# Performance work log

Hardware: AMD Instinct MI355X
Metric: run time of the kernel (lower is better)

## Reference

```python
import jax, jax.numpy as jnp
import numpy as np
import math

B, C, H, W = 512, 64, 8, 8
E, NH, MEM = 64, 8, 8          # embed_dim, num_heads, mem_n
HD = E // NH                   # head_dim
THD = H * W * HD               # tot_head_dim = 512
AMB = 5.0                      # attn_mask_b
LN_EPS = 1e-5


def conv2d(x, w, b):
    y = jax.lax.conv_general_dilated(x, w, (1, 1), 'SAME',
                                     dimension_numbers=('NCHW', 'OIHW', 'NCHW'))
    return y + b[None, :, None, None]


def setup_inputs() -> dict:
    key = jax.random.key(0)
    ks = jax.random.split(key, 14)
    r = lambda k, s, sc=1.0: jax.random.normal(k, s, dtype=jnp.float32) * sc
    return {
        'input': r(ks[0], (B, C, H, W)),
        'h_cur': r(ks[1], (B, E, H, W)),
        'c_cur': r(ks[2], (B, E, H, W)),
        'concat_k': r(ks[3], (B, MEM, NH, THD)),
        'concat_v': r(ks[4], (B, MEM, NH, THD)),
        'attn_mask': jax.random.randint(ks[5], (B * NH, 1, MEM), 0, 2).astype(bool),
        'conv_w': r(ks[6], (5 * E, C + E, 3, 3), 0.05),
        'conv_b': jnp.zeros((5 * E,), jnp.float32),
        'proj_w': r(ks[7], (3 * E, C, 3, 3), 0.05),
        'proj_b': jnp.zeros((3 * E,), jnp.float32),
        'out_w': r(ks[8], (E, E, 3, 3), 0.05),
        'out_b': jnp.zeros((E,), jnp.float32),
        'ln_w': jnp.ones((E, H, W), jnp.float32),
        'ln_b': jnp.zeros((E, H, W), jnp.float32),
        'pos_w': r(ks[9], (MEM, H * W * E), 0.02),
        'pos_b': jax.random.uniform(ks[10], (MEM, NH), jnp.float32, -0.1, 0.1),
    }


def _cell(input, h_cur, c_cur, concat_k, concat_v, attn_mask,
          conv_w, conv_b, proj_w, proj_b, out_w, out_b, ln_w, ln_b, pos_w, pos_b):
    # ConvLSTM gates
    combined = jnp.concatenate([input, h_cur], axis=1)          # [B, C+E, H, W]
    cc = conv2d(combined, conv_w, conv_b)                       # [B, 5E, H, W]
    cc_i, cc_f, cc_o, cc_g, cc_a = jnp.split(cc, 5, axis=1)
    i = jax.nn.sigmoid(cc_i)
    f = jax.nn.sigmoid(cc_f)
    o = jax.nn.sigmoid(cc_o)
    g = jnp.tanh(cc_g)
    a = jax.nn.sigmoid(cc_a)
    c_next = f * c_cur + i * g

    # attention over growing memory
    kqv = conv2d(input, proj_w, proj_b)                         # [B, 3E, H, W]
    k, q, v = jnp.split(kqv, 3, axis=1)
    # [B, E, H, W] -> [B*NH, 1, THD] (contiguous split of E into NH heads)
    resh = lambda x: x.reshape(B * NH, 1, THD)
    k, q, v = resh(k), resh(q), resh(v)
    q_scaled = q / math.sqrt(THD)

    # prior memory: [B, MEM, NH, THD] -> [B*NH, MEM-1, THD]
    def mem_resh(m):
        return jnp.transpose(m[:, 1:], (1, 0, 2, 3)).reshape(MEM - 1, B * NH, THD).transpose(1, 0, 2)
    k_full = jnp.concatenate([mem_resh(concat_k), k], axis=1)   # [B*NH, MEM, THD]
    v_full = jnp.concatenate([mem_resh(concat_v), v], axis=1)

    # learned positional key offsets / score biases
    pos_w_e = jnp.broadcast_to(pos_w[:, None, :], (MEM, B, H * W * E)) \
                 .reshape(MEM, B * NH, THD).transpose(1, 0, 2)  # [B*NH, MEM, THD]
    pos_b_e = jnp.broadcast_to(pos_b[:, None, :], (MEM, B, NH)) \
                 .reshape(MEM, B * NH).T                        # [B*NH, MEM]
    k_full = k_full + pos_w_e

    # additive mask: -inf where masked, last slot forced to +attn_mask_b
    mask = jnp.where(attn_mask, -jnp.inf, 0.0).astype(q.dtype)  # [B*NH, 1, MEM]
    mask = mask.at[:, :, -1].set(AMB)

    scores = mask + jnp.einsum('bqd,bkd->bqk', q_scaled, k_full) + pos_b_e[:, None, :]
    w = jax.nn.softmax(scores, axis=-1)                         # [B*NH, 1, MEM]
    attn = jnp.einsum('bqk,bkd->bqd', w, v_full)                # [B*NH, 1, THD]
    attn = attn.reshape(B, E, H, W)

    out = conv2d(attn, out_w, out_b) + input[:, :E]
    # LayerNorm over (E, H, W)
    mu = jnp.mean(out, axis=(1, 2, 3), keepdims=True)
    var = jnp.mean((out - mu) ** 2, axis=(1, 2, 3), keepdims=True)
    out = (out - mu) / jnp.sqrt(var + LN_EPS) * ln_w[None] + ln_b[None]

    c_next = c_next + a * jnp.tanh(out)
    h_next = o * jnp.tanh(c_next)

    ret = lambda m: m.transpose(1, 0, 2).reshape(MEM, B, NH, THD).transpose(1, 0, 2, 3)
    return h_next, c_next, ret(k_full), ret(v_full)


def reference(input, h_cur, c_cur, concat_k, concat_v, attn_mask,
              conv_w, conv_b, proj_w, proj_b, out_w, out_b, ln_w, ln_b, pos_w, pos_b):
    return _cell(input, h_cur, c_cur, concat_k, concat_v, attn_mask,
                 conv_w, conv_b, proj_w, proj_b, out_w, out_b, ln_w, ln_b, pos_w, pos_b)
```

## Files before the change

### kernel.cpp

```cpp
#include <hip/hip_runtime.h>

typedef short short8 __attribute__((ext_vector_type(8)));
typedef __bf16 bf16x8 __attribute__((ext_vector_type(8)));
typedef float f32x4 __attribute__((ext_vector_type(4)));
typedef short s16x4 __attribute__((ext_vector_type(4)));
typedef unsigned u32x4 __attribute__((ext_vector_type(4)));

__device__ __forceinline__ short f2bf(float f) {
  unsigned u = __builtin_bit_cast(unsigned, f);
  u = (u + 0x7FFFu + ((u >> 16) & 1u)) >> 16;
  return (short)u;
}
__device__ __forceinline__ f32x4 mfma16(short8 a, short8 b, f32x4 c) {
  return __builtin_amdgcn_mfma_f32_16x16x32_bf16(
      __builtin_bit_cast(bf16x8, a), __builtin_bit_cast(bf16x8, b), c, 0, 0, 0);
}
__device__ __forceinline__ float sigm(float x) { return 1.0f / (1.0f + __expf(-x)); }
__device__ __forceinline__ float ftanh(float x) {
  return 1.0f - 2.0f / (1.0f + __expf(2.0f * x));
}
__device__ __forceinline__ f32x4 ld4(const float* p) { return *(const f32x4*)p; }
__device__ __forceinline__ void ntst4(float* p, f32x4 v) {
  __builtin_nontemporal_store(v, (f32x4*)p);
}
// ... 25 lines not shown
    }
    *(short8*)&out[(46080 + e) * 8] = v;
    return;
  }
  e -= 13824;
  {
    int kb8 = e / 64, n = e % 64;
    short8 v;
#pragma unroll
    for (int j = 0; j < 8; ++j) {
      int k = kb8 * 8 + j;
      int tap = k >> 6, ci = k & 63;
      v[j] = f2bf(w3[(n * 64 + ci) * 9 + tap]);
    }
    *(short8*)&out[(46080 + 13824 + e) * 8] = v;
  }
}

__launch_bounds__(512, 4)
__global__ void mid2_k(const float* __restrict__ input, const float* __restrict__ h_cur,
                       const float* __restrict__ c_cur, const float* __restrict__ ck,
                       const int* __restrict__ amask,
                       const float* __restrict__ conv_b, const float* __restrict__ proj_b,
                       const float* __restrict__ pos_w, const float* __restrict__ pos_b,
                       const short* __restrict__ pk1, const short* __restrict__ pk2,
                       float* __restrict__ o_k, float* __restrict__ o_v,
                       float* __restrict__ ws_wt, float* __restrict__ ws_ct,
                       unsigned* __restrict__ ws_oa) {
  __shared__ short comb[12800];
  __shared__ float Xb[4160];
  __shared__ float Vx[4160];
  __shared__ float sc_lds[8];
  float* combf = (float*)comb;
  unsigned* Xbu = (unsigned*)Xb;

  const int tid = threadIdx.x;
  const int wave = tid >> 6, lane = tid & 63;
  const int col = lane & 15, g4 = lane >> 4;
  const int wc = wave >> 1, wm = wave & 1;
  const int ch = wc * 16 + col;

  if (blockIdx.x < 512) {
    const int b = blockIdx.x;
    const int hd = wave;
    const int d0 = lane * 4, d1 = (lane + 64) * 4;
    if (tid < 8) sc_lds[tid] = 0.f;

#pragma unroll
    for (int i = 0; i < 2; ++i) {
      int idx = (tid + 512 * i) * 4;
      int c = idx >> 6, p0 = idx & 63;
      f32x4 vi = ld4(&input[b * 4096 + idx]);
#pragma unroll
      for (int j = 0; j < 4; ++j) {
        int p = p0 + j;
        int pp = ((p >> 3) + 1) * 10 + (p & 7) + 1;
        comb[pp * 64 + ((c + pp * 8) & 63)] = f2bf(vi[j]);
      }
    }
    for (int i = tid; i < 2304; i += 512) {
      int pr = i >> 6, c = i & 63;
      int pp = (pr < 10) ? pr
               : (pr < 20) ? (80 + pr)
               : (pr < 28) ? ((pr - 19) * 10)
                           : ((pr - 27) * 10 + 9);
      comb[pp * 64 + c] = 0;
    }
    __syncthreads();

    f32x4 acc2[2][3];
#pragma unroll
    for (int m = 0; m < 2; ++m)
#pragma unroll
      for (int g = 0; g < 3; ++g) acc2[m][g] = (f32x4){0.f, 0.f, 0.f, 0.f};
    short8 bb2[3];
#pragma unroll
    for (int g = 0; g < 3; ++g)
      bb2[g] = *(const short8*)&pk2[((g4)*192 + g * 64 + ch) * 8];
    for (int s = 0; s < 18; ++s) {
      short8 bbn[3];
      if (s < 17) {
        int kb8 = (s + 1) * 4 + g4;
#pragma unroll
        for (int g = 0; g < 3; ++g)
          bbn[g] = *(const short8*)&pk2[(kb8 * 192 + g * 64 + ch) * 8];
      }
      int tap = s >> 1, cib = s & 1;
      int kh = tap / 3, kw = tap % 3;
      short8 a[2];
#pragma unroll
      for (int m = 0; m < 2; ++m) {
        int p = (wm * 2 + m) * 16 + col;
        int pp = ((p >> 3) + kh) * 10 + (p & 7) + kw;
        int slot = (cib * 32 + g4 * 8 + pp * 8) & 63;
        a[m] = *(const short8*)&comb[pp * 64 + slot];
      }
#pragma unroll
      for (int m = 0; m < 2; ++m)
#pragma unroll
        for (int g = 0; g < 3; ++g) acc2[m][g] = mfma16(a[m], bb2[g], acc2[m][g]);
      if (s < 17) {
#pragma unroll
        for (int g = 0; g < 3; ++g) bb2[g] = bbn[g];
      }
    }

    float kreg[8], qreg[8], vreg[8], part7 = 0.f;
    {
      float pb0 = proj_b[ch], pb1 = proj_b[64 + ch], pb2 = proj_b[128 + ch];
      const float rsq = 0.044194173824159216f;
#pragma unroll
      for (int m = 0; m < 2; ++m)
#pragma unroll
        for (int r = 0; r < 4; ++r) {
          int p = (wm * 2 + m) * 16 + g4 * 4 + r;
          float kf = acc2[m][0][r] + pb0 + pos_w[7 * 4096 + ch * 64 + p];
          float qf = (acc2[m][1][r] + pb1) * rsq;
          float vf = acc2[m][2][r] + pb2;
          kreg[m * 4 + r] = kf;
          qreg[m * 4 + r] = qf;
          vreg[m * 4 + r] = vf;
          part7 = fmaf(qf, kf, part7);
        }
    }
    atomicAdd(&sc_lds[ch >> 3], part7);

    int msks[7];
    float pbv[7];
#pragma unroll
    for (int m = 0; m < 7; ++m) {
      msks[m] = amask[(b * 8 + hd) * 8 + m];
      pbv[m] = pos_b[m * 8 + hd];
    }

    __syncthreads();

#pragma unroll
    for (int m = 0; m < 2; ++m)
#pragma unroll
      for (int r = 0; r < 4; ++r) {
        int p = (wm * 2 + m) * 16 + g4 * 4 + r;
        combf[ch * 65 + p] = kreg[m * 4 + r];
        Xb[ch * 65 + p] = qreg[m * 4 + r];
        Vx[ch * 65 + p] = vreg[m * 4 + r];
      }
    __syncthreads();

    const size_t base7 = (size_t)(b * 64 + 56) * 512;
#pragma unroll
    for (int i = 0; i < 2; ++i) {
      int idx = (tid + 512 * i) * 4;
      int c = idx >> 6, p0 = idx & 63;
      f32x4 kq, vq;
#pragma unroll
      for (int j = 0; j < 4; ++j) {
        kq[j] = combf[c * 65 + p0 + j];
        vq[j] = Vx[c * 65 + p0 + j];
      }
      ntst4(&o_k[base7 + idx], kq);
      *(f32x4*)&o_v[base7 + idx] = vq;
    }
    const int cs0 = d0 >> 6, po0 = d0 & 63, cs1 = d1 >> 6, po1 = d1 & 63;
    f32x4 q0, q1;
#pragma unroll
    for (int j = 0; j < 4; ++j) {
      q0[j] = Xb[(hd * 8 + cs0) * 65 + po0 + j];
      q1[j] = Xb[(hd * 8 + cs1) * 65 + po1 + j];
    }
    float sc7 = sc_lds[hd] + pos_b[7 * 8 + hd] + 5.0f;

    float scv[8];
    scv[7] = sc7;
#pragma unroll
    for (int m = 0; m < 7; ++m) {
      const float* kp = ck + ((size_t)((b * 8 + m + 1) * 8 + hd)) * 512;
      const float* pw = pos_w + m * 4096 + hd * 512;
      f32x4 k0 = ld4(kp + d0) + ld4(pw + d0);
      f32x4 k1 = ld4(kp + d1) + ld4(pw + d1);
      float* dst = o_k + ((size_t)((b * 8 + m) * 8 + hd)) * 512;
      ntst4(dst + d0, k0);
      ntst4(dst + d1, k1);
      float part = 0.f;
#pragma unroll
      for (int j = 0; j < 4; ++j) {
        part = fmaf(q0[j], k0[j], part);
        part = fmaf(q1[j], k1[j], part);
      }
#pragma unroll
      for (int off = 32; off >= 1; off >>= 1) part += __shfl_xor(part, off);
      scv[m] = part + pbv[m] + (msks[m] ? -__builtin_inff() : 0.0f);
    }

    float mx = scv[0];
#pragma unroll
    for (int m = 1; m < 8; ++m) mx = fmaxf(mx, scv[m]);
    float w[8], s = 0.f;
#pragma unroll
    for (int m = 0; m < 8; ++m) {
      w[m] = __expf(scv[m] - mx);
      s += w[m];
    }
    float inv = 1.0f / s;
    if (lane == 0) {
#pragma unroll
      for (int m = 0; m < 8; ++m)
        ws_wt[(size_t)b * 64 + hd * 8 + m] = w[m] * inv;
    }
  } else {
    const int b = blockIdx.x - 512;
#pragma unroll
    for (int i = 0; i < 2; ++i) {
      int idx = (tid + 512 * i) * 4;
      int c = idx >> 6, p0 = idx & 63;
      f32x4 vi = ld4(&input[b * 4096 + idx]);
      f32x4 vh = ld4(&h_cur[b * 4096 + idx]);
      f32x4 vc = ld4(&c_cur[b * 4096 + idx]);
#pragma unroll
      for (int j = 0; j < 4; ++j) {
        int p = p0 + j;
        int pp = ((p >> 3) + 1) * 10 + (p & 7) + 1;
        comb[pp * 128 + ((c + pp * 8) & 127)] = f2bf(vi[j]);
        comb[pp * 128 + ((c + 64 + pp * 8) & 127)] = f2bf(vh[j]);
        Xb[c * 65 + p] = vc[j];
      }
    }
    for (int i = tid; i < 4608; i += 512) {
      int pr = i >> 7, c = i & 127;
      int pp = (pr < 10) ? pr
               : (pr < 20) ? (80 + pr)
               : (pr < 28) ? ((pr - 19) * 10)
                           : ((pr - 27) * 10 + 9);
      comb[pp * 128 + c] = 0;
    }
    __syncthreads();

    f32x4 acc1[2][5];
#pragma unroll
    for (int m = 0; m < 2; ++m)
#pragma unroll
      for (int g = 0; g < 5; ++g) acc1[m][g] = (f32x4){0.f, 0.f, 0.f, 0.f};
    short8 bb1[5];
#pragma unroll
    for (int g = 0; g < 5; ++g)
      bb1[g] = *(const short8*)&pk1[((g4)*320 + g * 64 + ch) * 8];
    for (int s = 0; s < 36; ++s) {
      short8 bbn[5];
      if (s < 35) {
        int kb8 = (s + 1) * 4 + g4;
#pragma unroll
        for (int g = 0; g < 5; ++g)
          bbn[g] = *(const short8*)&pk1[(kb8 * 320 + g * 64 + ch) * 8];
      }
      int tap = s >> 2, cib = s & 3;
      int kh = tap / 3, kw = tap % 3;
      short8 a[2];
#pragma unroll
      for (int m = 0; m < 2; ++m) {
        int p = (wm * 2 + m) * 16 + col;
        int pp = ((p >> 3) + kh) * 10 + (p & 7) + kw;
        int slot = (cib * 32 + g4 * 8 + pp * 8) & 127;
        a[m] = *(const short8*)&comb[pp * 128 + slot];
      }
#pragma unroll
      for (int m = 0; m < 2; ++m)
#pragma unroll
        for (int g = 0; g < 5; ++g) acc1[m][g] = mfma16(a[m], bb1[g], acc1[m][g]);
      if (s < 35) {
#pragma unroll
        for (int g = 0; g < 5; ++g) bb1[g] = bbn[g];
      }
    }

    float ctv[8];
    unsigned oav[8];
    {
      float bi0 = conv_b[ch], bi1 = conv_b[64 + ch], bi2 = conv_b[128 + ch];
      float bi3 = conv_b[192 + ch], bi4 = conv_b[256 + ch];
#pragma unroll
      for (int m = 0; m < 2; ++m)
#pragma unroll
        for (int r = 0; r < 4; ++r) {
          int p = (wm * 2 + m) * 16 + g4 * 4 + r;
          float iv = sigm(acc1[m][0][r] + bi0);
          float fv = sigm(acc1[m][1][r] + bi1);
          float ov = sigm(acc1[m][2][r] + bi2);
          float gv = ftanh(acc1[m][3][r] + bi3);
          float av = sigm(acc1[m][4][r] + bi4);
          ctv[m * 4 + r] = fv * Xb[ch * 65 + p] + iv * gv;
          oav[m * 4 + r] = ((unsigned)(unsigned short)f2bf(av) << 16) |
                           (unsigned)(unsigned short)f2bf(ov);
        }
    }
    __syncthreads();
#pragma unroll
    for (int m = 0; m < 2; ++m)
#pragma unroll
      for (int r = 0; r < 4; ++r) {
        int p = (wm * 2 + m) * 16 + g4 * 4 + r;
        combf[ch * 65 + p] = ctv[m * 4 + r];
        Xbu[ch * 65 + p] = oav[m * 4 + r];
      }
    __syncthreads();
#pragma unroll
    for (int i = 0; i < 2; ++i) {
      int idx = (tid + 512 * i) * 4;
      int c = idx >> 6, p0 = idx & 63;
      f32x4 cq;
      u32x4 oq;
#pragma unroll
      for (int j = 0; j < 4; ++j) {
        cq[j] = combf[c * 65 + p0 + j];
        oq[j] = Xbu[c * 65 + p0 + j];
      }
      *(f32x4*)&ws_ct[(size_t)b * 4096 + idx] = cq;
      *(u32x4*)&ws_oa[(size_t)b * 4096 + idx] = oq;
    }
  }
}

__launch_bounds__(512, 4)
__global__ void tail_k(const float* __restrict__ input, const float* __restrict__ cv,
                       const float* __restrict__ ws_wt,
                       const float* __restrict__ ws_ct,
                       const unsigned* __restrict__ ws_oa,
                       const float* __restrict__ out_b,
                       const float* __restrict__ ln_w, const float* __restrict__ ln_b,
                       const short* __restrict__ pk3,
                       float* __restrict__ o_h, float* __restrict__ o_c,
                       float* __restrict__ o_v) {
  __shared__ short comb[8320];
  __shared__ float Xb[4160];
  __shared__ float wt_s[64];
  __shared__ float red[16];
  float* combf = (float*)comb;
  unsigned* Xbu = (unsigned*)Xb;

  const int b = blockIdx.x;
  const int tid = threadIdx.x;
  const int wave = tid >> 6, lane = tid & 63;
  const int col = lane & 15, g4 = lane >> 4;
  const int wc = wave >> 1, wm = wave & 1;
  const int ch = wc * 16 + col;
  const int hd = wave;
  const int d0 = lane * 4, d1 = (lane + 64) * 4;

  f32x4 ctr[2];
  u32x4 oar[2];
#pragma unroll
  for (int i = 0; i < 2; ++i) {
    int idx = (tid + 512 * i) * 4;
    ctr[i] = ld4(&ws_ct[(size_t)b * 4096 + idx]);
    oar[i] = *(const u32x4*)&ws_oa[(size_t)b * 4096 + idx];
  }
  if (tid < 64) wt_s[tid] = ws_wt[(size_t)b * 64 + tid];

#pragma unroll
  for (int i = 0; i < 2; ++i) {
    int idx = (tid + 512 * i) * 4;
    int c = idx >> 6, p0 = idx & 63;
    f32x4 vi = ld4(&input[b * 4096 + idx]);
#pragma unroll
    for (int j = 0; j < 4; ++j) Xb[c * 65 + p0 + j] = vi[j];
  }
  for (int i = tid; i < 2304; i += 512) {
    int pr = i >> 6, c = i & 63;
    int pp = (pr < 10) ? pr
             : (pr < 20) ? (80 + pr)
             : (pr < 28) ? ((pr - 19) * 10)
                         : ((pr - 27) * 10 + 9);
    comb[pp * 64 + c] = 0;
  }
  __syncthreads();

  float wv[8];
#pragma unroll
  for (int m = 0; m < 8; ++m) wv[m] = wt_s[hd * 8 + m];

  f32x4 a0 = (f32x4){0.f, 0.f, 0.f, 0.f};
  f32x4 a1 = (f32x4){0.f, 0.f, 0.f, 0.f};
#pragma unroll
  for (int m = 0; m < 7; ++m) {
    const float* vp = cv + ((size_t)((b * 8 + m + 1) * 8 + hd)) * 512;
    f32x4 v0 = ld4(vp + d0);
    f32x4 v1 = ld4(vp + d1);
    float* dst = o_v + ((size_t)((b * 8 + m) * 8 + hd)) * 512;
    ntst4(dst + d0, v0);
    ntst4(dst + d1, v1);
    a0 += v0 * wv[m];
    a1 += v1 * wv[m];
  }
  {
    const float* vp = o_v + ((size_t)((b * 8 + 7) * 8 + hd)) * 512;
    a0 += ld4(vp + d0) * wv[7];
    a1 += ld4(vp + d1) * wv[7];
  }
#pragma unroll
  for (int j = 0; j < 4; ++j) {
    int dA = d0 + j, dB = d1 + j;
    int cA = hd * 8 + (dA >> 6), pA = dA & 63;
    int cB = hd * 8 + (dB >> 6), pB = dB & 63;
    int ppA = ((pA >> 3) + 1) * 10 + (pA & 7) + 1;
    int ppB = ((pB >> 3) + 1) * 10 + (pB & 7) + 1;
    comb[ppA * 64 + ((cA + ppA * 8) & 63)] = f2bf(a0[j]);
    comb[ppB * 64 + ((cB + ppB * 8) & 63)] = f2bf(a1[j]);
  }
  __syncthreads();

  f32x4 acc3[2];
  acc3[0] = (f32x4){0.f, 0.f, 0.f, 0.f};
  acc3[1] = (f32x4){0.f, 0.f, 0.f, 0.f};
  short8 bb3 = *(const short8*)&pk3[((g4)*64 + ch) * 8];
  for (int s = 0; s < 18; ++s) {
    short8 bbn;
    if (s < 17) {
      int kb8 = (s + 1) * 4 + g4;
      bbn = *(const short8*)&pk3[(kb8 * 64 + ch) * 8];
    }
    int tap = s >> 1, cib = s & 1;
    int kh = tap / 3, kw = tap % 3;
    short8 a[2];
#pragma unroll
    for (int m = 0; m < 2; ++m) {
      int p = (wm * 2 + m) * 16 + col;
      int pp = ((p >> 3) + kh) * 10 + (p & 7) + kw;
      int slot = (cib * 32 + g4 * 8 + pp * 8) & 63;
      a[m] = *(const short8*)&comb[pp * 64 + slot];
    }
#pragma unroll
    for (int m = 0; m < 2; ++m) acc3[m] = mfma16(a[m], bb3, acc3[m]);
    if (s < 17) bb3 = bbn;
  }

  float ov_[8], s1 = 0.f, s2 = 0.f;
  {
    float ob = out_b[ch];
#pragma unroll
    for (int m = 0; m < 2; ++m)
#pragma unroll
      for (int r = 0; r < 4; ++r) {
        int p = (wm * 2 + m) * 16 + g4 * 4 + r;
        float v = acc3[m][r] + ob + Xb[ch * 65 + p];
        ov_[m * 4 + r] = v;
        s1 += v;
        s2 += v * v;
      }
  }
#pragma unroll
  for (int off = 32; off >= 1; off >>= 1) {
    s1 += __shfl_xor(s1, off);
    s2 += __shfl_xor(s2, off);
  }
  if (lane == 0) { red[wave] = s1; red[8 + wave] = s2; }
  __syncthreads();
  float ts1 = 0.f, ts2 = 0.f;
#pragma unroll
  for (int w = 0; w < 8; ++w) { ts1 += red[w]; ts2 += red[8 + w]; }
  float mu = ts1 * (1.0f / 4096.0f);
  float var = ts2 * (1.0f / 4096.0f) - mu * mu;
  float rstd = rsqrtf(var + 1e-5f);

#pragma unroll
  for (int i = 0; i < 2; ++i) {
    int idx = (tid + 512 * i) * 4;
    int c = idx >> 6, p0 = idx & 63;
#pragma unroll
    for (int j = 0; j < 4; ++j) {
      combf[c * 65 + p0 + j] = ctr[i][j];
      Xbu[c * 65 + p0 + j] = oar[i][j];
    }
  }
  __syncthreads();

#pragma unroll
  for (int m = 0; m < 2; ++m)
#pragma unroll
    for (int r = 0; r < 4; ++r) {
      int p = (wm * 2 + m) * 16 + g4 * 4 + r;
      float ct = combf[ch * 65 + p];
      unsigned u = Xbu[ch * 65 + p];
      float og = __builtin_bit_cast(float, u << 16);
      float ag = __builtin_bit_cast(float, u & 0xffff0000u);
      float oln = (ov_[m * 4 + r] - mu) * rstd * ln_w[ch * 64 + p] + ln_b[ch * 64 + p];
      float cn = ct + ag * ftanh(oln);
      float hv = og * ftanh(cn);
      combf[ch * 65 + p] = hv;
      Xb[ch * 65 + p] = cn;
    }
  __syncthreads();
#pragma unroll
  for (int i = 0; i < 2; ++i) {
    int idx = (tid + 512 * i) * 4;
    int c = idx >> 6, p0 = idx & 63;
    f32x4 hq, cq;
#pragma unroll
    for (int j = 0; j < 4; ++j) {
      hq[j] = combf[c * 65 + p0 + j];
      cq[j] = Xb[c * 65 + p0 + j];
    }
    *(f32x4*)&o_h[b * 4096 + idx] = hq;
    *(f32x4*)&o_c[b * 4096 + idx] = cq;
  }
}

__launch_bounds__(512, 4)
__global__ void kqv_k(const float* __restrict__ input,
                      const float* __restrict__ proj_b,
                      const float* __restrict__ pos_w,
                      const short* __restrict__ pk2,
                      float* __restrict__ q_out, float* __restrict__ o_k,
                      float* __restrict__ o_v) {
  __shared__ short comb[6400];
  __shared__ float Xk[4160], Xq[4160], Xv[4160];
  const int b = blockIdx.x;
  const int tid = threadIdx.x;
  const int wave = tid >> 6, lane = tid & 63;
// ... 74 lines not shown
  const size_t base7 = (size_t)(b * 64 + 56) * 512;
#pragma unroll
  for (int i = 0; i < 2; ++i) {
    int idx = (tid + 512 * i) * 4;
    int c = idx >> 6, p0 = idx & 63;
    f32x4 kq, qq, vq;
#pragma unroll
    for (int j = 0; j < 4; ++j) {
      kq[j] = Xk[c * 65 + p0 + j];
      qq[j] = Xq[c * 65 + p0 + j];
      vq[j] = Xv[c * 65 + p0 + j];
    }
    *(f32x4*)&o_k[base7 + idx] = kq;
    *(f32x4*)&q_out[(size_t)b * 4096 + idx] = qq;
    *(f32x4*)&o_v[base7 + idx] = vq;
  }
}

__launch_bounds__(64, 4)
__global__ void attn_k(const float* __restrict__ ck, const float* __restrict__ cv,
                       const int* __restrict__ amask,
                       const float* __restrict__ pos_w,
                       const float* __restrict__ pos_b,
                       const float* __restrict__ q_in,
                       float* __restrict__ o_k, float* __restrict__ o_v,
                       float* __restrict__ attn_out) {
  const int b = blockIdx.x >> 3;
  const int hd = blockIdx.x & 7;
  const int lane = threadIdx.x;
  const int d0 = lane * 4, d1 = (lane + 64) * 4;
// ... 288 lines not shown
  const float* out_b  = (const float*)d_in[11];
  const float* ln_w   = (const float*)d_in[12];
  const float* ln_b   = (const float*)d_in[13];
  const float* pos_w  = (const float*)d_in[14];
  const float* pos_b  = (const float*)d_in[15];

  char* ws = (char*)d_ws;
  short* pk = (short*)ws;
  float* o_h = (float*)d_out;
  float* o_c = o_h + 2097152;
  float* o_k = o_h + 4194304;
  float* o_v = o_h + 20971520;

  pack_w<<<252, 256, 0, stream>>>(conv_w, proj_w, out_w, pk);

  if (ws_size >= (24u << 20)) {
    float* ws_wt = (float*)(ws + (2u << 20));
    float* ws_ct = (float*)(ws + (8u << 20));
    unsigned* ws_oa = (unsigned*)(ws + (16u << 20));
    mid2_k<<<1024, 512, 0, stream>>>(input, h_cur, c_cur, ck, amask,
                                     conv_b, proj_b, pos_w, pos_b,
                                     pk, pk + 368640,
                                     o_k, o_v, ws_wt, ws_ct, ws_oa);
    tail_k<<<512, 512, 0, stream>>>(input, cv, ws_wt, ws_ct, ws_oa,
                                    out_b, ln_w, ln_b, pk + 479232,
                                    o_h, o_c, o_v);
  } else {
    kqv_k<<<512, 512, 0, stream>>>(input, proj_b, pos_w, pk + 368640,
                                   o_h, o_k, o_v);
    attn_k<<<4096, 64, 0, stream>>>(ck, cv, amask, pos_w, pos_b, o_h,
                                    o_k, o_v, o_c);
    cell2_k<<<512, 512, 0, stream>>>(input, h_cur, c_cur, o_c,
                                     conv_b, out_b, ln_w, ln_b,
                                     pk, pk + 479232, o_h, o_c);
  }
}
```

Baseline: 99.34 us.

## Split fused mid kernel into separate kqv, gate and key-streaming kernels

Replaces the combined mid2_k kernel with separate kernels. kqv_k writes q to workspace, gate_k computes the ConvLSTM gates, and kstream_k streams the old keys and computes raw attention scores. The softmax over scores moves into tail_k. The aim is to stop the memory-bound key copy from sitting in the same heterogeneous launch as the MFMA-heavy gate convolution, so each kernel's resources and occupancy can be tuned on their own. The cost is two more launches and extra workspace traffic for q and the scores, and the workspace requirement rises to 32 MB.

```diff
diff --git a/kernel.cpp b/kernel.cpp
--- a/kernel.cpp
+++ b/kernel.cpp
@@ -63,491 +63,6 @@
       v[j] = f2bf(w3[(n * 64 + ci) * 9 + tap]);
     }
     *(short8*)&out[(46080 + 13824 + e) * 8] = v;
-  }
-}
-
-__launch_bounds__(512, 4)
-__global__ void mid2_k(const float* __restrict__ input, const float* __restrict__ h_cur,
-                       const float* __restrict__ c_cur, const float* __restrict__ ck,
-                       const int* __restrict__ amask,
-                       const float* __restrict__ conv_b, const float* __restrict__ proj_b,
-                       const float* __restrict__ pos_w, const float* __restrict__ pos_b,
-                       const short* __restrict__ pk1, const short* __restrict__ pk2,
-                       float* __restrict__ o_k, float* __restrict__ o_v,
-                       float* __restrict__ ws_wt, float* __restrict__ ws_ct,
-                       unsigned* __restrict__ ws_oa) {
-  __shared__ short comb[12800];
-  __shared__ float Xb[4160];
-  __shared__ float Vx[4160];
-  __shared__ float sc_lds[8];
-  float* combf = (float*)comb;
-  unsigned* Xbu = (unsigned*)Xb;
-
-  const int tid = threadIdx.x;
-  const int wave = tid >> 6, lane = tid & 63;
-  const int col = lane & 15, g4 = lane >> 4;
-  const int wc = wave >> 1, wm = wave & 1;
-  const int ch = wc * 16 + col;
-
-  if (blockIdx.x < 512) {
-    const int b = blockIdx.x;
-    const int hd = wave;
-    const int d0 = lane * 4, d1 = (lane + 64) * 4;
-    if (tid < 8) sc_lds[tid] = 0.f;
-
-#pragma unroll
-    for (int i = 0; i < 2; ++i) {
-      int idx = (tid + 512 * i) * 4;
-      int c = idx >> 6, p0 = idx & 63;
-      f32x4 vi = ld4(&input[b * 4096 + idx]);
-#pragma unroll
-      for (int j = 0; j < 4; ++j) {
-        int p = p0 + j;
-        int pp = ((p >> 3) + 1) * 10 + (p & 7) + 1;
-        comb[pp * 64 + ((c + pp * 8) & 63)] = f2bf(vi[j]);
-      }
-    }
-    for (int i = tid; i < 2304; i += 512) {
-      int pr = i >> 6, c = i & 63;
-      int pp = (pr < 10) ? pr
-               : (pr < 20) ? (80 + pr)
-               : (pr < 28) ? ((pr - 19) * 10)
-                           : ((pr - 27) * 10 + 9);
-      comb[pp * 64 + c] = 0;
-    }
-    __syncthreads();
-
-    f32x4 acc2[2][3];
-#pragma unroll
-    for (int m = 0; m < 2; ++m)
-#pragma unroll
-      for (int g = 0; g < 3; ++g) acc2[m][g] = (f32x4){0.f, 0.f, 0.f, 0.f};
-    short8 bb2[3];
-#pragma unroll
-    for (int g = 0; g < 3; ++g)
-      bb2[g] = *(const short8*)&pk2[((g4)*192 + g * 64 + ch) * 8];
-    for (int s = 0; s < 18; ++s) {
-      short8 bbn[3];
-      if (s < 17) {
-        int kb8 = (s + 1) * 4 + g4;
-#pragma unroll
-        for (int g = 0; g < 3; ++g)
-          bbn[g] = *(const short8*)&pk2[(kb8 * 192 + g * 64 + ch) * 8];
-      }
-      int tap = s >> 1, cib = s & 1;
-      int kh = tap / 3, kw = tap % 3;
-      short8 a[2];
-#pragma unroll
-      for (int m = 0; m < 2; ++m) {
-        int p = (wm * 2 + m) * 16 + col;
-        int pp = ((p >> 3) + kh) * 10 + (p & 7) + kw;
-        int slot = (cib * 32 + g4 * 8 + pp * 8) & 63;
-        a[m] = *(const short8*)&comb[pp * 64 + slot];
-      }
-#pragma unroll
-      for (int m = 0; m < 2; ++m)
-#pragma unroll
-        for (int g = 0; g < 3; ++g) acc2[m][g] = mfma16(a[m], bb2[g], acc2[m][g]);
-      if (s < 17) {
-#pragma unroll
-        for (int g = 0; g < 3; ++g) bb2[g] = bbn[g];
-      }
-    }
-
-    float kreg[8], qreg[8], vreg[8], part7 = 0.f;
-    {
-      float pb0 = proj_b[ch], pb1 = proj_b[64 + ch], pb2 = proj_b[128 + ch];
-      const float rsq = 0.044194173824159216f;
-#pragma unroll
-      for (int m = 0; m < 2; ++m)
-#pragma unroll
-        for (int r = 0; r < 4; ++r) {
-          int p = (wm * 2 + m) * 16 + g4 * 4 + r;
-          float kf = acc2[m][0][r] + pb0 + pos_w[7 * 4096 + ch * 64 + p];
-          float qf = (acc2[m][1][r] + pb1) * rsq;
-          float vf = acc2[m][2][r] + pb2;
-          kreg[m * 4 + r] = kf;
-          qreg[m * 4 + r] = qf;
-          vreg[m * 4 + r] = vf;
-          part7 = fmaf(qf, kf, part7);
-        }
-    }
-    atomicAdd(&sc_lds[ch >> 3], part7);
-
-    int msks[7];
-    float pbv[7];
-#pragma unroll
-    for (int m = 0; m < 7; ++m) {
-      msks[m] = amask[(b * 8 + hd) * 8 + m];
-      pbv[m] = pos_b[m * 8 + hd];
-    }
-
-    __syncthreads();
-
-#pragma unroll
-    for (int m = 0; m < 2; ++m)
-#pragma unroll
-      for (int r = 0; r < 4; ++r) {
-        int p = (wm * 2 + m) * 16 + g4 * 4 + r;
-        combf[ch * 65 + p] = kreg[m * 4 + r];
-        Xb[ch * 65 + p] = qreg[m * 4 + r];
-        Vx[ch * 65 + p] = vreg[m * 4 + r];
-      }
-    __syncthreads();
-
-    const size_t base7 = (size_t)(b * 64 + 56) * 512;
-#pragma unroll
-    for (int i = 0; i < 2; ++i) {
-      int idx = (tid + 512 * i) * 4;
-      int c = idx >> 6, p0 = idx & 63;
-      f32x4 kq, vq;
-#pragma unroll
-      for (int j = 0; j < 4; ++j) {
-        kq[j] = combf[c * 65 + p0 + j];
-        vq[j] = Vx[c * 65 + p0 + j];
-      }
-      ntst4(&o_k[base7 + idx], kq);
-      *(f32x4*)&o_v[base7 + idx] = vq;
-    }
-    const int cs0 = d0 >> 6, po0 = d0 & 63, cs1 = d1 >> 6, po1 = d1 & 63;
-    f32x4 q0, q1;
-#pragma unroll
-    for (int j = 0; j < 4; ++j) {
-      q0[j] = Xb[(hd * 8 + cs0) * 65 + po0 + j];
-      q1[j] = Xb[(hd * 8 + cs1) * 65 + po1 + j];
-    }
-    float sc7 = sc_lds[hd] + pos_b[7 * 8 + hd] + 5.0f;
-
-    float scv[8];
-    scv[7] = sc7;
-#pragma unroll
-    for (int m = 0; m < 7; ++m) {
-      const float* kp = ck + ((size_t)((b * 8 + m + 1) * 8 + hd)) * 512;
-      const float* pw = pos_w + m * 4096 + hd * 512;
-      f32x4 k0 = ld4(kp + d0) + ld4(pw + d0);
-      f32x4 k1 = ld4(kp + d1) + ld4(pw + d1);
-      float* dst = o_k + ((size_t)((b * 8 + m) * 8 + hd)) * 512;
-      ntst4(dst + d0, k0);
-      ntst4(dst + d1, k1);
-      float part = 0.f;
-#pragma unroll
-      for (int j = 0; j < 4; ++j) {
-        part = fmaf(q0[j], k0[j], part);
-        part = fmaf(q1[j], k1[j], part);
-      }
-#pragma unroll
-      for (int off = 32; off >= 1; off >>= 1) part += __shfl_xor(part, off);
-      scv[m] = part + pbv[m] + (msks[m] ? -__builtin_inff() : 0.0f);
-    }
-
-    float mx = scv[0];
-#pragma unroll
-    for (int m = 1; m < 8; ++m) mx = fmaxf(mx, scv[m]);
-    float w[8], s = 0.f;
-#pragma unroll
-    for (int m = 0; m < 8; ++m) {
-      w[m] = __expf(scv[m] - mx);
-      s += w[m];
-    }
-    float inv = 1.0f / s;
-    if (lane == 0) {
-#pragma unroll
-      for (int m = 0; m < 8; ++m)
-        ws_wt[(size_t)b * 64 + hd * 8 + m] = w[m] * inv;
-    }
-  } else {
-    const int b = blockIdx.x - 512;
-#pragma unroll
-    for (int i = 0; i < 2; ++i) {
-      int idx = (tid + 512 * i) * 4;
-      int c = idx >> 6, p0 = idx & 63;
-      f32x4 vi = ld4(&input[b * 4096 + idx]);
-      f32x4 vh = ld4(&h_cur[b * 4096 + idx]);
-      f32x4 vc = ld4(&c_cur[b * 4096 + idx]);
-#pragma unroll
-      for (int j = 0; j < 4; ++j) {
-        int p = p0 + j;
-        int pp = ((p >> 3) + 1) * 10 + (p & 7) + 1;
-        comb[pp * 128 + ((c + pp * 8) & 127)] = f2bf(vi[j]);
-        comb[pp * 128 + ((c + 64 + pp * 8) & 127)] = f2bf(vh[j]);
-        Xb[c * 65 + p] = vc[j];
-      }
-    }
-    for (int i = tid; i < 4608; i += 512) {
-      int pr = i >> 7, c = i & 127;
-      int pp = (pr < 10) ? pr
-               : (pr < 20) ? (80 + pr)
-               : (pr < 28) ? ((pr - 19) * 10)
-                           : ((pr - 27) * 10 + 9);
-      comb[pp * 128 + c] = 0;
-    }
-    __syncthreads();
-
-    f32x4 acc1[2][5];
-#pragma unroll
-    for (int m = 0; m < 2; ++m)
-#pragma unroll
-      for (int g = 0; g < 5; ++g) acc1[m][g] = (f32x4){0.f, 0.f, 0.f, 0.f};
-    short8 bb1[5];
-#pragma unroll
-    for (int g = 0; g < 5; ++g)
-      bb1[g] = *(const short8*)&pk1[((g4)*320 + g * 64 + ch) * 8];
-    for (int s = 0; s < 36; ++s) {
-      short8 bbn[5];
-      if (s < 35) {
-        int kb8 = (s + 1) * 4 + g4;
-#pragma unroll
-        for (int g = 0; g < 5; ++g)
-          bbn[g] = *(const short8*)&pk1[(kb8 * 320 + g * 64 + ch) * 8];
-      }
-      int tap = s >> 2, cib = s & 3;
-      int kh = tap / 3, kw = tap % 3;
-      short8 a[2];
-#pragma unroll
-      for (int m = 0; m < 2; ++m) {
-        int p = (wm * 2 + m) * 16 + col;
-        int pp = ((p >> 3) + kh) * 10 + (p & 7) + kw;
-        int slot = (cib * 32 + g4 * 8 + pp * 8) & 127;
-        a[m] = *(const short8*)&comb[pp * 128 + slot];
-      }
-#pragma unroll
-      for (int m = 0; m < 2; ++m)
-#pragma unroll
-        for (int g = 0; g < 5; ++g) acc1[m][g] = mfma16(a[m], bb1[g], acc1[m][g]);
-      if (s < 35) {
-#pragma unroll
-        for (int g = 0; g < 5; ++g) bb1[g] = bbn[g];
-      }
-    }
-
-    float ctv[8];
-    unsigned oav[8];
-    {
-      float bi0 = conv_b[ch], bi1 = conv_b[64 + ch], bi2 = conv_b[128 + ch];
-      float bi3 = conv_b[192 + ch], bi4 = conv_b[256 + ch];
-#pragma unroll
-      for (int m = 0; m < 2; ++m)
-#pragma unroll
-        for (int r = 0; r < 4; ++r) {
-          int p = (wm * 2 + m) * 16 + g4 * 4 + r;
-          float iv = sigm(acc1[m][0][r] + bi0);
-          float fv = sigm(acc1[m][1][r] + bi1);
-          float ov = sigm(acc1[m][2][r] + bi2);
-          float gv = ftanh(acc1[m][3][r] + bi3);
-          float av = sigm(acc1[m][4][r] + bi4);
-          ctv[m * 4 + r] = fv * Xb[ch * 65 + p] + iv * gv;
-          oav[m * 4 + r] = ((unsigned)(unsigned short)f2bf(av) << 16) |
-                           (unsigned)(unsigned short)f2bf(ov);
-        }
-    }
-    __syncthreads();
-#pragma unroll
-    for (int m = 0; m < 2; ++m)
-#pragma unroll
-      for (int r = 0; r < 4; ++r) {
-        int p = (wm * 2 + m) * 16 + g4 * 4 + r;
-        combf[ch * 65 + p] = ctv[m * 4 + r];
-        Xbu[ch * 65 + p] = oav[m * 4 + r];
-      }
-    __syncthreads();
-#pragma unroll
-    for (int i = 0; i < 2; ++i) {
-      int idx = (tid + 512 * i) * 4;
-      int c = idx >> 6, p0 = idx & 63;
-      f32x4 cq;
-      u32x4 oq;
-#pragma unroll
-      for (int j = 0; j < 4; ++j) {
-        cq[j] = combf[c * 65 + p0 + j];
-        oq[j] = Xbu[c * 65 + p0 + j];
-      }
-      *(f32x4*)&ws_ct[(size_t)b * 4096 + idx] = cq;
-      *(u32x4*)&ws_oa[(size_t)b * 4096 + idx] = oq;
-    }
-  }
-}
-
-__launch_bounds__(512, 4)
-__global__ void tail_k(const float* __restrict__ input, const float* __restrict__ cv,
-                       const float* __restrict__ ws_wt,
-                       const float* __restrict__ ws_ct,
-                       const unsigned* __restrict__ ws_oa,
-                       const float* __restrict__ out_b,
-                       const float* __restrict__ ln_w, const float* __restrict__ ln_b,
-                       const short* __restrict__ pk3,
-                       float* __restrict__ o_h, float* __restrict__ o_c,
-                       float* __restrict__ o_v) {
-  __shared__ short comb[8320];
-  __shared__ float Xb[4160];
-  __shared__ float wt_s[64];
-  __shared__ float red[16];
-  float* combf = (float*)comb;
-  unsigned* Xbu = (unsigned*)Xb;
-
-  const int b = blockIdx.x;
-  const int tid = threadIdx.x;
-  const int wave = tid >> 6, lane = tid & 63;
-  const int col = lane & 15, g4 = lane >> 4;
-  const int wc = wave >> 1, wm = wave & 1;
-  const int ch = wc * 16 + col;
-  const int hd = wave;
-  const int d0 = lane * 4, d1 = (lane + 64) * 4;
-
-  f32x4 ctr[2];
-  u32x4 oar[2];
-#pragma unroll
-  for (int i = 0; i < 2; ++i) {
-    int idx = (tid + 512 * i) * 4;
-    ctr[i] = ld4(&ws_ct[(size_t)b * 4096 + idx]);
-    oar[i] = *(const u32x4*)&ws_oa[(size_t)b * 4096 + idx];
-  }
-  if (tid < 64) wt_s[tid] = ws_wt[(size_t)b * 64 + tid];
-
-#pragma unroll
-  for (int i = 0; i < 2; ++i) {
-    int idx = (tid + 512 * i) * 4;
-    int c = idx >> 6, p0 = idx & 63;
-    f32x4 vi = ld4(&input[b * 4096 + idx]);
-#pragma unroll
-    for (int j = 0; j < 4; ++j) Xb[c * 65 + p0 + j] = vi[j];
-  }
-  for (int i = tid; i < 2304; i += 512) {
-    int pr = i >> 6, c = i & 63;
-    int pp = (pr < 10) ? pr
-             : (pr < 20) ? (80 + pr)
-             : (pr < 28) ? ((pr - 19) * 10)
-                         : ((pr - 27) * 10 + 9);
-    comb[pp * 64 + c] = 0;
-  }
-  __syncthreads();
-
-  float wv[8];
-#pragma unroll
-  for (int m = 0; m < 8; ++m) wv[m] = wt_s[hd * 8 + m];
-
-  f32x4 a0 = (f32x4){0.f, 0.f, 0.f, 0.f};
-  f32x4 a1 = (f32x4){0.f, 0.f, 0.f, 0.f};
-#pragma unroll
-  for (int m = 0; m < 7; ++m) {
-    const float* vp = cv + ((size_t)((b * 8 + m + 1) * 8 + hd)) * 512;
-    f32x4 v0 = ld4(vp + d0);
-    f32x4 v1 = ld4(vp + d1);
-    float* dst = o_v + ((size_t)((b * 8 + m) * 8 + hd)) * 512;
-    ntst4(dst + d0, v0);
-    ntst4(dst + d1, v1);
-    a0 += v0 * wv[m];
-    a1 += v1 * wv[m];
-  }
-  {
-    const float* vp = o_v + ((size_t)((b * 8 + 7) * 8 + hd)) * 512;
-    a0 += ld4(vp + d0) * wv[7];
-    a1 += ld4(vp + d1) * wv[7];
-  }
-#pragma unroll
-  for (int j = 0; j < 4; ++j) {
-    int dA = d0 + j, dB = d1 + j;
-    int cA = hd * 8 + (dA >> 6), pA = dA & 63;
-    int cB = hd * 8 + (dB >> 6), pB = dB & 63;
-    int ppA = ((pA >> 3) + 1) * 10 + (pA & 7) + 1;
-    int ppB = ((pB >> 3) + 1) * 10 + (pB & 7) + 1;
-    comb[ppA * 64 + ((cA + ppA * 8) & 63)] = f2bf(a0[j]);
-    comb[ppB * 64 + ((cB + ppB * 8) & 63)] = f2bf(a1[j]);
-  }
-  __syncthreads();
-
-  f32x4 acc3[2];
-  acc3[0] = (f32x4){0.f, 0.f, 0.f, 0.f};
-  acc3[1] = (f32x4){0.f, 0.f, 0.f, 0.f};
-  short8 bb3 = *(const short8*)&pk3[((g4)*64 + ch) * 8];
-  for (int s = 0; s < 18; ++s) {
-    short8 bbn;
-    if (s < 17) {
-      int kb8 = (s + 1) * 4 + g4;
-      bbn = *(const short8*)&pk3[(kb8 * 64 + ch) * 8];
-    }
-    int tap = s >> 1, cib = s & 1;
-    int kh = tap / 3, kw = tap % 3;
-    short8 a[2];
-#pragma unroll
-    for (int m = 0; m < 2; ++m) {
-      int p = (wm * 2 + m) * 16 + col;
-      int pp = ((p >> 3) + kh) * 10 + (p & 7) + kw;
-      int slot = (cib * 32 + g4 * 8 + pp * 8) & 63;
-      a[m] = *(const short8*)&comb[pp * 64 + slot];
-    }
-#pragma unroll
-    for (int m = 0; m < 2; ++m) acc3[m] = mfma16(a[m], bb3, acc3[m]);
-    if (s < 17) bb3 = bbn;
-  }
-
-  float ov_[8], s1 = 0.f, s2 = 0.f;
-  {
-    float ob = out_b[ch];
-#pragma unroll
-    for (int m = 0; m < 2; ++m)
-#pragma unroll
-      for (int r = 0; r < 4; ++r) {
-        int p = (wm * 2 + m) * 16 + g4 * 4 + r;
-        float v = acc3[m][r] + ob + Xb[ch * 65 + p];
-        ov_[m * 4 + r] = v;
-        s1 += v;
-        s2 += v * v;
-      }
-  }
-#pragma unroll
-  for (int off = 32; off >= 1; off >>= 1) {
-    s1 += __shfl_xor(s1, off);
-    s2 += __shfl_xor(s2, off);
-  }
-  if (lane == 0) { red[wave] = s1; red[8 + wave] = s2; }
-  __syncthreads();
-  float ts1 = 0.f, ts2 = 0.f;
-#pragma unroll
-  for (int w = 0; w < 8; ++w) { ts1 += red[w]; ts2 += red[8 + w]; }
-  float mu = ts1 * (1.0f / 4096.0f);
-  float var = ts2 * (1.0f / 4096.0f) - mu * mu;
-  float rstd = rsqrtf(var + 1e-5f);
-
-#pragma unroll
-  for (int i = 0; i < 2; ++i) {
-    int idx = (tid + 512 * i) * 4;
-    int c = idx >> 6, p0 = idx & 63;
-#pragma unroll
-    for (int j = 0; j < 4; ++j) {
-      combf[c * 65 + p0 + j] = ctr[i][j];
-      Xbu[c * 65 + p0 + j] = oar[i][j];
-    }
-  }
-  __syncthreads();
-
-#pragma unroll
-  for (int m = 0; m < 2; ++m)
-#pragma unroll
-    for (int r = 0; r < 4; ++r) {
-      int p = (wm * 2 + m) * 16 + g4 * 4 + r;
-      float ct = combf[ch * 65 + p];
-      unsigned u = Xbu[ch * 65 + p];
-      float og = __builtin_bit_cast(float, u << 16);
-      float ag = __builtin_bit_cast(float, u & 0xffff0000u);
-      float oln = (ov_[m * 4 + r] - mu) * rstd * ln_w[ch * 64 + p] + ln_b[ch * 64 + p];
-      float cn = ct + ag * ftanh(oln);
-      float hv = og * ftanh(cn);
-      combf[ch * 65 + p] = hv;
-      Xb[ch * 65 + p] = cn;
-    }
-  __syncthreads();
-#pragma unroll
-  for (int i = 0; i < 2; ++i) {
-    int idx = (tid + 512 * i) * 4;
-    int c = idx >> 6, p0 = idx & 63;
-    f32x4 hq, cq;
-#pragma unroll
-    for (int j = 0; j < 4; ++j) {
-      hq[j] = combf[c * 65 + p0 + j];
-      cq[j] = Xb[c * 65 + p0 + j];
-    }
-    *(f32x4*)&o_h[b * 4096 + idx] = hq;
-    *(f32x4*)&o_c[b * 4096 + idx] = cq;
   }
 }
 
@@ -652,6 +167,395 @@
     *(f32x4*)&o_k[base7 + idx] = kq;
     *(f32x4*)&q_out[(size_t)b * 4096 + idx] = qq;
     *(f32x4*)&o_v[base7 + idx] = vq;
+  }
+}
+
+__launch_bounds__(512, 4)
+__global__ void kstream_k(const float* __restrict__ ck,
+                          const float* __restrict__ pos_w,
+                          const float* __restrict__ ws_q,
+                          float* __restrict__ o_k,
+                          float* __restrict__ ws_sc) {
+  const int b = blockIdx.x;
+  const int tid = threadIdx.x;
+  const int hd = tid >> 6, lane = tid & 63;
+  const int d0 = lane * 4, d1 = (lane + 64) * 4;
+
+  f32x4 q0 = ld4(&ws_q[(size_t)b * 4096 + hd * 512 + d0]);
+  f32x4 q1 = ld4(&ws_q[(size_t)b * 4096 + hd * 512 + d1]);
+
+  float part[8];
+#pragma unroll
+  for (int m = 0; m < 8; ++m) part[m] = 0.f;
+
+#pragma unroll
+  for (int m = 0; m < 7; ++m) {
+    const float* src = ck + ((size_t)((b * 8 + m + 1) * 8 + hd)) * 512;
+    const float* pw = pos_w + m * 4096 + hd * 512;
+    f32x4 k0 = ld4(src + d0) + ld4(pw + d0);
+    f32x4 k1 = ld4(src + d1) + ld4(pw + d1);
+    float* dst = o_k + ((size_t)((b * 8 + m) * 8 + hd)) * 512;
+    ntst4(dst + d0, k0);
+    ntst4(dst + d1, k1);
+#pragma unroll
+    for (int j = 0; j < 4; ++j) {
+      part[m] = fmaf(q0[j], k0[j], part[m]);
+      part[m] = fmaf(q1[j], k1[j], part[m]);
+    }
+  }
+  {
+    const float* src = o_k + ((size_t)((b * 8 + 7) * 8 + hd)) * 512;
+    f32x4 k0 = ld4(src + d0);
+    f32x4 k1 = ld4(src + d1);
+#pragma unroll
+    for (int j = 0; j < 4; ++j) {
+      part[7] = fmaf(q0[j], k0[j], part[7]);
+      part[7] = fmaf(q1[j], k1[j], part[7]);
+    }
+  }
+#pragma unroll
+  for (int m = 0; m < 8; ++m) {
+#pragma unroll
+    for (int off = 32; off >= 1; off >>= 1)
+      part[m] += __shfl_xor(part[m], off);
+  }
+  if (lane == 0) {
+#pragma unroll
+    for (int m = 0; m < 8; ++m)
+      ws_sc[(size_t)b * 64 + hd * 8 + m] = part[m];
+  }
+}
+
+__launch_bounds__(512, 4)
+__global__ void gate_k(const float* __restrict__ input, const float* __restrict__ h_cur,
+                       const float* __restrict__ c_cur,
+                       const float* __restrict__ conv_b,
+                       const short* __restrict__ pk1,
+                       float* __restrict__ ws_ct, unsigned* __restrict__ ws_oa) {
+  __shared__ short comb[12800];
+  __shared__ float Xb[4160];
+  float* combf = (float*)comb;
+  unsigned* Xbu = (unsigned*)Xb;
+
+  const int b = blockIdx.x;
+  const int tid = threadIdx.x;
+  const int wave = tid >> 6, lane = tid & 63;
+  const int col = lane & 15, g4 = lane >> 4;
+  const int wc = wave >> 1, wm = wave & 1;
+  const int ch = wc * 16 + col;
+
+#pragma unroll
+  for (int i = 0; i < 2; ++i) {
+    int idx = (tid + 512 * i) * 4;
+    int c = idx >> 6, p0 = idx & 63;
+    f32x4 vi = ld4(&input[b * 4096 + idx]);
+    f32x4 vh = ld4(&h_cur[b * 4096 + idx]);
+    f32x4 vc = ld4(&c_cur[b * 4096 + idx]);
+#pragma unroll
+    for (int j = 0; j < 4; ++j) {
+      int p = p0 + j;
+      int pp = ((p >> 3) + 1) * 10 + (p & 7) + 1;
+      comb[pp * 128 + ((c + pp * 8) & 127)] = f2bf(vi[j]);
+      comb[pp * 128 + ((c + 64 + pp * 8) & 127)] = f2bf(vh[j]);
+      Xb[c * 65 + p] = vc[j];
+    }
+  }
+  for (int i = tid; i < 4608; i += 512) {
+    int pr = i >> 7, c = i & 127;
+    int pp = (pr < 10) ? pr
+             : (pr < 20) ? (80 + pr)
+             : (pr < 28) ? ((pr - 19) * 10)
+                         : ((pr - 27) * 10 + 9);
+    comb[pp * 128 + c] = 0;
+  }
+  __syncthreads();
+
+  f32x4 acc1[2][5];
+#pragma unroll
+  for (int m = 0; m < 2; ++m)
+#pragma unroll
+    for (int g = 0; g < 5; ++g) acc1[m][g] = (f32x4){0.f, 0.f, 0.f, 0.f};
+  short8 bb1[5];
+#pragma unroll
+  for (int g = 0; g < 5; ++g)
+    bb1[g] = *(const short8*)&pk1[((g4)*320 + g * 64 + ch) * 8];
+  for (int s = 0; s < 36; ++s) {
+    short8 bbn[5];
+    if (s < 35) {
+      int kb8 = (s + 1) * 4 + g4;
+#pragma unroll
+      for (int g = 0; g < 5; ++g)
+        bbn[g] = *(const short8*)&pk1[(kb8 * 320 + g * 64 + ch) * 8];
+    }
+    int tap = s >> 2, cib = s & 3;
+    int kh = tap / 3, kw = tap % 3;
+    short8 a[2];
+#pragma unroll
+    for (int m = 0; m < 2; ++m) {
+      int p = (wm * 2 + m) * 16 + col;
+      int pp = ((p >> 3) + kh) * 10 + (p & 7) + kw;
+      int slot = (cib * 32 + g4 * 8 + pp * 8) & 127;
+      a[m] = *(const short8*)&comb[pp * 128 + slot];
+    }
+#pragma unroll
+    for (int m = 0; m < 2; ++m)
+#pragma unroll
+      for (int g = 0; g < 5; ++g) acc1[m][g] = mfma16(a[m], bb1[g], acc1[m][g]);
+    if (s < 35) {
+#pragma unroll
+      for (int g = 0; g < 5; ++g) bb1[g] = bbn[g];
+    }
+  }
+
+  float ctv[8];
+  unsigned oav[8];
+  {
+    float bi0 = conv_b[ch], bi1 = conv_b[64 + ch], bi2 = conv_b[128 + ch];
+    float bi3 = conv_b[192 + ch], bi4 = conv_b[256 + ch];
+#pragma unroll
+    for (int m = 0; m < 2; ++m)
+#pragma unroll
+      for (int r = 0; r < 4; ++r) {
+        int p = (wm * 2 + m) * 16 + g4 * 4 + r;
+        float iv = sigm(acc1[m][0][r] + bi0);
+        float fv = sigm(acc1[m][1][r] + bi1);
+        float ov = sigm(acc1[m][2][r] + bi2);
+        float gv = ftanh(acc1[m][3][r] + bi3);
+        float av = sigm(acc1[m][4][r] + bi4);
+        ctv[m * 4 + r] = fv * Xb[ch * 65 + p] + iv * gv;
+        oav[m * 4 + r] = ((unsigned)(unsigned short)f2bf(av) << 16) |
+                         (unsigned)(unsigned short)f2bf(ov);
+      }
+  }
+  __syncthreads();
+#pragma unroll
+  for (int m = 0; m < 2; ++m)
+#pragma unroll
+    for (int r = 0; r < 4; ++r) {
+      int p = (wm * 2 + m) * 16 + g4 * 4 + r;
+      combf[ch * 65 + p] = ctv[m * 4 + r];
+      Xbu[ch * 65 + p] = oav[m * 4 + r];
+    }
+  __syncthreads();
+#pragma unroll
+  for (int i = 0; i < 2; ++i) {
+    int idx = (tid + 512 * i) * 4;
+    int c = idx >> 6, p0 = idx & 63;
+    f32x4 cq;
+    u32x4 oq;
+#pragma unroll
+    for (int j = 0; j < 4; ++j) {
+      cq[j] = combf[c * 65 + p0 + j];
+      oq[j] = Xbu[c * 65 + p0 + j];
+    }
+    *(f32x4*)&ws_ct[(size_t)b * 4096 + idx] = cq;
+    *(u32x4*)&ws_oa[(size_t)b * 4096 + idx] = oq;
+  }
+}
+
+__launch_bounds__(512, 4)
+__global__ void tail_k(const float* __restrict__ input, const float* __restrict__ cv,
+                       const float* __restrict__ ws_sc,
+                       const float* __restrict__ ws_ct,
+                       const unsigned* __restrict__ ws_oa,
+                       const int* __restrict__ amask,
+                       const float* __restrict__ pos_b,
+                       const float* __restrict__ out_b,
+                       const float* __restrict__ ln_w, const float* __restrict__ ln_b,
+                       const short* __restrict__ pk3,
+                       float* __restrict__ o_h, float* __restrict__ o_c,
+                       float* __restrict__ o_v) {
+  __shared__ short comb[8320];
+  __shared__ float Xb[4160];
+  __shared__ float wt_s[64];
+  __shared__ float red[16];
+  float* combf = (float*)comb;
+  unsigned* Xbu = (unsigned*)Xb;
+
+  const int b = blockIdx.x;
+  const int tid = threadIdx.x;
+  const int wave = tid >> 6, lane = tid & 63;
+  const int col = lane & 15, g4 = lane >> 4;
+  const int wc = wave >> 1, wm = wave & 1;
+  const int ch = wc * 16 + col;
+  const int hd = wave;
+  const int d0 = lane * 4, d1 = (lane + 64) * 4;
+
+  f32x4 ctr[2];
+  u32x4 oar[2];
+#pragma unroll
+  for (int i = 0; i < 2; ++i) {
+    int idx = (tid + 512 * i) * 4;
+    ctr[i] = ld4(&ws_ct[(size_t)b * 4096 + idx]);
+    oar[i] = *(const u32x4*)&ws_oa[(size_t)b * 4096 + idx];
+  }
+  if (tid < 8) {
+    const int head = tid;
+    float scv[8];
+#pragma unroll
+    for (int m = 0; m < 7; ++m)
+      scv[m] = ws_sc[(size_t)b * 64 + head * 8 + m] + pos_b[m * 8 + head] +
+               (amask[(b * 8 + head) * 8 + m] ? -__builtin_inff() : 0.0f);
+    scv[7] = ws_sc[(size_t)b * 64 + head * 8 + 7] + pos_b[56 + head] + 5.0f;
+    float mx = scv[0];
+#pragma unroll
+    for (int m = 1; m < 8; ++m) mx = fmaxf(mx, scv[m]);
+    float w[8], s = 0.f;
+#pragma unroll
+    for (int m = 0; m < 8; ++m) {
+      w[m] = __expf(scv[m] - mx);
+      s += w[m];
+    }
+    float inv = 1.0f / s;
+#pragma unroll
+    for (int m = 0; m < 8; ++m) wt_s[head * 8 + m] = w[m] * inv;
+  }
+
+#pragma unroll
+  for (int i = 0; i < 2; ++i) {
+    int idx = (tid + 512 * i) * 4;
+    int c = idx >> 6, p0 = idx & 63;
+    f32x4 vi = ld4(&input[b * 4096 + idx]);
+#pragma unroll
+    for (int j = 0; j < 4; ++j) Xb[c * 65 + p0 + j] = vi[j];
+  }
+  for (int i = tid; i < 2304; i += 512) {
+    int pr = i >> 6, c = i & 63;
+    int pp = (pr < 10) ? pr
+             : (pr < 20) ? (80 + pr)
+             : (pr < 28) ? ((pr - 19) * 10)
+                         : ((pr - 27) * 10 + 9);
+    comb[pp * 64 + c] = 0;
+  }
+  __syncthreads();
+
+  float wv[8];
+#pragma unroll
+  for (int m = 0; m < 8; ++m) wv[m] = wt_s[hd * 8 + m];
+
+  f32x4 a0 = (f32x4){0.f, 0.f, 0.f, 0.f};
+  f32x4 a1 = (f32x4){0.f, 0.f, 0.f, 0.f};
+#pragma unroll
+  for (int m = 0; m < 7; ++m) {
+    const float* vp = cv + ((size_t)((b * 8 + m + 1) * 8 + hd)) * 512;
+    f32x4 v0 = ld4(vp + d0);
+    f32x4 v1 = ld4(vp + d1);
+    float* dst = o_v + ((size_t)((b * 8 + m) * 8 + hd)) * 512;
+    ntst4(dst + d0, v0);
+    ntst4(dst + d1, v1);
+    a0 += v0 * wv[m];
+    a1 += v1 * wv[m];
+  }
+  {
+    const float* vp = o_v + ((size_t)((b * 8 + 7) * 8 + hd)) * 512;
+    a0 += ld4(vp + d0) * wv[7];
+    a1 += ld4(vp + d1) * wv[7];
+  }
+#pragma unroll
+  for (int j = 0; j < 4; ++j) {
+    int dA = d0 + j, dB = d1 + j;
+    int cA = hd * 8 + (dA >> 6), pA = dA & 63;
+    int cB = hd * 8 + (dB >> 6), pB = dB & 63;
+    int ppA = ((pA >> 3) + 1) * 10 + (pA & 7) + 1;
+    int ppB = ((pB >> 3) + 1) * 10 + (pB & 7) + 1;
+    comb[ppA * 64 + ((cA + ppA * 8) & 63)] = f2bf(a0[j]);
+    comb[ppB * 64 + ((cB + ppB * 8) & 63)] = f2bf(a1[j]);
+  }
+  __syncthreads();
+
+  f32x4 acc3[2];
+  acc3[0] = (f32x4){0.f, 0.f, 0.f, 0.f};
+  acc3[1] = (f32x4){0.f, 0.f, 0.f, 0.f};
+  short8 bb3 = *(const short8*)&pk3[((g4)*64 + ch) * 8];
+  for (int s = 0; s < 18; ++s) {
+    short8 bbn;
+    if (s < 17) {
+      int kb8 = (s + 1) * 4 + g4;
+      bbn = *(const short8*)&pk3[(kb8 * 64 + ch) * 8];
+    }
+    int tap = s >> 1, cib = s & 1;
+    int kh = tap / 3, kw = tap % 3;
+    short8 a[2];
+#pragma unroll
+    for (int m = 0; m < 2; ++m) {
+      int p = (wm * 2 + m) * 16 + col;
+      int pp = ((p >> 3) + kh) * 10 + (p & 7) + kw;
+      int slot = (cib * 32 + g4 * 8 + pp * 8) & 63;
+      a[m] = *(const short8*)&comb[pp * 64 + slot];
+    }
+#pragma unroll
+    for (int m = 0; m < 2; ++m) acc3[m] = mfma16(a[m], bb3, acc3[m]);
+    if (s < 17) bb3 = bbn;
+  }
+
+  float ov_[8], s1 = 0.f, s2 = 0.f;
+  {
+    float ob = out_b[ch];
+#pragma unroll
+    for (int m = 0; m < 2; ++m)
+#pragma unroll
+      for (int r = 0; r < 4; ++r) {
+        int p = (wm * 2 + m) * 16 + g4 * 4 + r;
+        float v = acc3[m][r] + ob + Xb[ch * 65 + p];
+        ov_[m * 4 + r] = v;
+        s1 += v;
+        s2 += v * v;
+      }
+  }
+#pragma unroll
+  for (int off = 32; off >= 1; off >>= 1) {
+    s1 += __shfl_xor(s1, off);
+    s2 += __shfl_xor(s2, off);
+  }
+  if (lane == 0) { red[wave] = s1; red[8 + wave] = s2; }
+  __syncthreads();
+  float ts1 = 0.f, ts2 = 0.f;
+#pragma unroll
+  for (int w = 0; w < 8; ++w) { ts1 += red[w]; ts2 += red[8 + w]; }
+  float mu = ts1 * (1.0f / 4096.0f);
+  float var = ts2 * (1.0f / 4096.0f) - mu * mu;
+  float rstd = rsqrtf(var + 1e-5f);
+
+#pragma unroll
+  for (int i = 0; i < 2; ++i) {
+    int idx = (tid + 512 * i) * 4;
+    int c = idx >> 6, p0 = idx & 63;
+#pragma unroll
+    for (int j = 0; j < 4; ++j) {
+      combf[c * 65 + p0 + j] = ctr[i][j];
+      Xbu[c * 65 + p0 + j] = oar[i][j];
+    }
+  }
+  __syncthreads();
+
+#pragma unroll
+  for (int m = 0; m < 2; ++m)
+#pragma unroll
+    for (int r = 0; r < 4; ++r) {
+      int p = (wm * 2 + m) * 16 + g4 * 4 + r;
+      float ct = combf[ch * 65 + p];
+      unsigned u = Xbu[ch * 65 + p];
+      float og = __builtin_bit_cast(float, u << 16);
+      float ag = __builtin_bit_cast(float, u & 0xffff0000u);
+      float oln = (ov_[m * 4 + r] - mu) * rstd * ln_w[ch * 64 + p] + ln_b[ch * 64 + p];
+      float cn = ct + ag * ftanh(oln);
+      float hv = og * ftanh(cn);
+      combf[ch * 65 + p] = hv;
+      Xb[ch * 65 + p] = cn;
+    }
+  __syncthreads();
+#pragma unroll
+  for (int i = 0; i < 2; ++i) {
+    int idx = (tid + 512 * i) * 4;
+    int c = idx >> 6, p0 = idx & 63;
+    f32x4 hq, cq;
+#pragma unroll
+    for (int j = 0; j < 4; ++j) {
+      hq[j] = combf[c * 65 + p0 + j];
+      cq[j] = Xb[c * 65 + p0 + j];
+    }
+    *(f32x4*)&o_h[b * 4096 + idx] = hq;
+    *(f32x4*)&o_c[b * 4096 + idx] = cq;
   }
 }
 
@@ -970,17 +874,19 @@
 
   pack_w<<<252, 256, 0, stream>>>(conv_w, proj_w, out_w, pk);
 
-  if (ws_size >= (24u << 20)) {
-    float* ws_wt = (float*)(ws + (2u << 20));
-    float* ws_ct = (float*)(ws + (8u << 20));
-    unsigned* ws_oa = (unsigned*)(ws + (16u << 20));
-    mid2_k<<<1024, 512, 0, stream>>>(input, h_cur, c_cur, ck, amask,
-                                     conv_b, proj_b, pos_w, pos_b,
-                                     pk, pk + 368640,
-                                     o_k, o_v, ws_wt, ws_ct, ws_oa);
-    tail_k<<<512, 512, 0, stream>>>(input, cv, ws_wt, ws_ct, ws_oa,
-                                    out_b, ln_w, ln_b, pk + 479232,
-                                    o_h, o_c, o_v);
+  if (ws_size >= (32u << 20)) {
+    float* ws_sc = (float*)(ws + (2u << 20));
+    float* ws_q  = (float*)(ws + (4u << 20));
+    float* ws_ct = (float*)(ws + (16u << 20));
+    unsigned* ws_oa = (unsigned*)(ws + (24u << 20));
+    kqv_k<<<512, 512, 0, stream>>>(input, proj_b, pos_w, pk + 368640,
+                                   ws_q, o_k, o_v);
+    gate_k<<<512, 512, 0, stream>>>(input, h_cur, c_cur, conv_b, pk,
+                                    ws_ct, ws_oa);
+    kstream_k<<<512, 512, 0, stream>>>(ck, pos_w, ws_q, o_k, ws_sc);
+    tail_k<<<512, 512, 0, stream>>>(input, cv, ws_sc, ws_ct, ws_oa,
+                                    amask, pos_b, out_b, ln_w, ln_b,
+                                    pk + 479232, o_h, o_c, o_v);
   } else {
     kqv_k<<<512, 512, 0, stream>>>(input, proj_b, pos_w, pk + 368640,
                                    o_h, o_k, o_v);
```

Result: slower. 110.4 us (+11.1%).
